# Performance work log

Measured on AMD Instinct MI355X. Metric: run time of the kernel, lower is better.

The kernel has to match this reference:

```python
import jax, jax.numpy as jnp
import numpy as np

NUM_BINS = 8
TAIL = 3.0
MBW = 0.001  # min_bin_width
MBH = 0.001  # min_bin_height
MD = 0.001   # min_derivative


def _conv(x, w, b):
    y = jax.lax.conv_general_dilated(x, w, (1, 1), 'SAME',
                                     dimension_numbers=('NCHW', 'OIHW', 'NCHW'))
    return y + b[None, :, None, None]


def _convnet(x, w1, b1, w2, b2, w3, b3):
    h = jax.nn.relu(_conv(x, w1, b1))
    h = jax.nn.relu(_conv(h, w2, b2))
    return _conv(h, w3, b3)


def _rqs_forward(x, uw, uh, ud):
    # x: (N,), uw/uh: (N, num_bins), ud: (N, num_bins-1)
    nb = uw.shape[-1]
    inside = (x >= -TAIL) & (x <= TAIL)
    xin = jnp.clip(x, -TAIL, TAIL)
    # linear tails: pad derivatives so boundary slope == 1
    const = float(np.log(np.exp(1.0 - MD) - 1.0))
    ud = jnp.pad(ud, ((0, 0), (1, 1)), constant_values=const)

    widths = jax.nn.softmax(uw, axis=-1)
    widths = MBW + (1.0 - MBW * nb) * widths
    cumw = jnp.pad(jnp.cumsum(widths, axis=-1), ((0, 0), (1, 0)))
    cumw = 2.0 * TAIL * cumw - TAIL
    cumw = cumw.at[:, 0].set(-TAIL).at[:, -1].set(TAIL)
    widths = cumw[:, 1:] - cumw[:, :-1]

    heights = jax.nn.softmax(uh, axis=-1)
    heights = MBH + (1.0 - MBH * nb) * heights
    cumh = jnp.pad(jnp.cumsum(heights, axis=-1), ((0, 0), (1, 0)))
    cumh = 2.0 * TAIL * cumh - TAIL
    cumh = cumh.at[:, 0].set(-TAIL).at[:, -1].set(TAIL)
    heights = cumh[:, 1:] - cumh[:, :-1]

    deriv = MD + jax.nn.softplus(ud)  # (N, nb+1)

    # searchsorted: locate bin of each element
    idx = jnp.clip(jnp.sum((xin[:, None] >= cumw).astype(jnp.int32), axis=-1) - 1, 0, nb - 1)
    gather = lambda t: jnp.take_along_axis(t, idx[:, None], axis=-1)[:, 0]

    in_cw = gather(cumw)
    in_w = gather(widths)
    in_ch = gather(cumh)
    in_h = gather(heights)
    in_delta = gather(heights / widths)
    d0 = gather(deriv)
    d1 = gather(deriv[:, 1:])

    theta = (xin - in_cw) / in_w
    tom = theta * (1.0 - theta)
    numer = in_h * (in_delta * theta ** 2 + d0 * tom)
    denom = in_delta + (d0 + d1 - 2.0 * in_delta) * tom
    y = in_ch + numer / denom
    dnum = in_delta ** 2 * (d1 * theta ** 2 + 2.0 * in_delta * tom + d0 * (1.0 - theta) ** 2)
    lad = jnp.log(dnum) - 2.0 * jnp.log(denom)

    y = jnp.where(inside, y, x)
    lad = jnp.where(inside, lad, 0.0)
    return y, lad


def setup_inputs() -> dict:
    key = jax.random.key(0)
    ks = jax.random.split(key, 9)
    B, C, H, W = 32, 12, 64, 64
    hidden = 128
    cond_c = C // 3
    out_spline = C * (3 * NUM_BINS - 1)
    x = jax.random.normal(ks[0], (B, C, H, W), dtype=jnp.float32)
    logdet = jnp.zeros((B,), dtype=jnp.float32)
    conditioning = jax.random.normal(ks[1], (B, cond_c, H, W), dtype=jnp.float32)
    w1 = jax.random.normal(ks[2], (hidden, C + cond_c, 3, 3), dtype=jnp.float32) * 0.05
    b1 = jnp.zeros((hidden,), dtype=jnp.float32)
    w2 = jax.random.normal(ks[3], (hidden, hidden, 1, 1), dtype=jnp.float32) * 0.05
    b2 = jnp.zeros((hidden,), dtype=jnp.float32)
    w3 = jax.random.normal(ks[4], (out_spline, hidden, 3, 3), dtype=jnp.float32) * 0.01
    b3 = jnp.zeros((out_spline,), dtype=jnp.float32)
    return {"x": x, "logdet": logdet, "conditioning": conditioning,
            "w1": w1, "b1": b1, "w2": w2, "b2": b2, "w3": w3, "b3": b3}


def reference(x, logdet, conditioning, w1, b1, w2, b2, w3, b3):
    B, C, H, W = x.shape
    net_in = jnp.concatenate([x, conditioning], axis=1)
    params = _convnet(net_in, w1, b1, w2, b2, w3, b3)  # (B, C*(3nb-1), H, W)
    params = params.reshape(B, C, 3 * NUM_BINS - 1, H, W)
    params = params.transpose(0, 1, 3, 4, 2).reshape(B * C * H * W, 3 * NUM_BINS - 1)
    uw = params[:, :NUM_BINS]
    uh = params[:, NUM_BINS:2 * NUM_BINS]
    ud = params[:, 2 * NUM_BINS:]
    y_flat, lad_flat = _rqs_forward(x.reshape(-1), uw, uh, ud)
    y = y_flat.reshape(B, C, H, W)
    logdet_out = logdet + lad_flat.reshape(B, -1).sum(axis=1)
    return y, logdet_out
```

## Files before the change

kernel.cpp:

```cpp
#include <hip/hip_runtime.h>
#include <math.h>


#define NY   1572864

typedef _Float16 half8 __attribute__((ext_vector_type(8)));
typedef _Float16 half4 __attribute__((ext_vector_type(4)));
typedef float f32x4 __attribute__((ext_vector_type(4)));

#define ASYNC16(gsrc, ldst) \
  __builtin_amdgcn_global_load_lds((const __attribute__((address_space(1))) unsigned int*)(gsrc), \
                                   (__attribute__((address_space(3))) unsigned int*)(ldst), 16, 0, 0)

#define H2P_PLANE 4356
#define H2P_IDX(b, cc, pp) ((((size_t)(b) * 4 + (cc)) * H2P_PLANE + (pp)) << 5)
#define XH_IDX(b, pp) (((size_t)(b) * H2P_PLANE + (pp)) << 5)

__global__ __launch_bounds__(256) void prep_xh_k(
    const float* __restrict__ w1, const float* __restrict__ w2,
    const float* __restrict__ w3, _Float16* __restrict__ w1h,
    _Float16* __restrict__ w2h, _Float16* __restrict__ w3h,
    const float* __restrict__ logdet, float* __restrict__ ld_out,
    const float* __restrict__ x, const float* __restrict__ cond,
    _Float16* __restrict__ xh, _Float16* __restrict__ h2p)
{
    const int i = blockIdx.x * 256 + threadIdx.x;
    if (i < 36864) {
        int k = i & 31, oc = (i >> 5) & 127, t = i >> 12;
        w1h[i] = (_Float16)((k < 16) ? w1[(oc * 16 + k) * 9 + t] : 0.f);
    }
    if (i < 16384) {
        int km = i & 31, oc = (i >> 5) & 127, ks = i >> 12;
        w2h[i] = (_Float16)w2[oc * 128 + ks * 32 + km];
    }
    {
        int cim = i & 31;
        int oc = (i >> 5) % 288;
        int tc = i / (288 * 32);
        int t = tc >> 2, cc = tc & 3;
        int c = oc / 24, j = oc % 24;
        int ci = cc * 32 + cim;
        float v = (j < 23) ? w3[((c * 23 + j) * 128 + ci) * 9 + t] : 0.f;
        w3h[i] = (_Float16)v;
    }
    if (i < 32) ld_out[i] = logdet[i];

    if (i < 133120) {
        const int q = i & 3;
        const int rest = i >> 2;
        const int r = rest % 260;
        const int cc2 = (rest / 260) & 3;
        const int bb = rest / 1040;
        int pp;
        if (r < 66)       pp = r;
        else if (r < 132) pp = 65 * 66 + (r - 66);
        else if (r < 196) pp = (r - 131) * 66;
        else              pp = (r - 195) * 66 + 65;
        f32x4 z = {0.f, 0.f, 0.f, 0.f};
        *(f32x4*)(h2p + H2P_IDX(bb, cc2, pp) + q * 8) = z;
    }

    if (i < 139392) {
        const int b = i / H2P_PLANE, pp = i % H2P_PLANE;
        const int pr = pp / 66, pc = pp % 66;
        const bool interior = (pr >= 1) && (pr <= 64) && (pc >= 1) && (pc <= 64);
        _Float16 v[32];
#pragma unroll
        for (int ci = 0; ci < 32; ++ci) v[ci] = (_Float16)0.f;
        if (interior) {
            const int p = (pr - 1) * 64 + (pc - 1);
#pragma unroll
            for (int ci = 0; ci < 12; ++ci)
                v[ci] = (_Float16)x[((size_t)(b * 12 + ci) << 12) + p];
#pragma unroll
            for (int ci = 0; ci < 4; ++ci)
                v[12 + ci] = (_Float16)cond[((size_t)(b * 4 + ci) << 12) + p];
        }
        _Float16* dst = xh + ((size_t)i << 5);
#pragma unroll
        for (int q = 0; q < 4; ++q) *(f32x4*)(dst + q * 8) = *(f32x4*)(v + q * 8);
    }
}

__global__ __launch_bounds__(256, 2) void conv12_k(
    const _Float16* __restrict__ xh, const _Float16* __restrict__ w1h,
    const _Float16* __restrict__ w2h, const float* __restrict__ b1,
    const float* __restrict__ b2, _Float16* __restrict__ h2p)
{
    __shared__ __align__(16) char smem[74240];
    float* b2l = (float*)(smem + 73728);
    _Float16* h1l = (_Float16*)smem;

    const int tid = threadIdx.x;
    const int wv = tid >> 6, lane = tid & 63;
    const int row16 = lane & 15, quad = lane >> 4;
    const int prow = wv >> 1, colb = (wv & 1) << 5;
    const int bid = blockIdx.x;
    const int b = bid >> 5;
    const int pim0 = (bid & 31) << 7;
    const int h0 = pim0 >> 6;

    if (tid < 128) b2l[tid] = b2[tid];
#pragma unroll
    for (int k = 0; k < 18; ++k)
        ASYNC16(w1h + (size_t)(k * 256 + tid) * 8, smem + (k * 256 + wv * 64) * 16);

    f32x4 acc[2][8];
#pragma unroll
    for (int pt = 0; pt < 2; ++pt)
#pragma unroll
        for (int ot = 0; ot < 8; ++ot) acc[pt][ot] = (f32x4){0.f, 0.f, 0.f, 0.f};

    __syncthreads();
    const _Float16* wl = (const _Float16*)smem;

    for (int t = 0; t < 9; ++t) {
        const int dy = t / 3, dx = t % 3;
        const int pbase = (h0 + prow + dy) * 66 + dx + colb + row16;
        half8 bf[2], af[8];
#pragma unroll
        for (int pt = 0; pt < 2; ++pt)
            bf[pt] = *(const half8*)(xh + XH_IDX(b, pbase + pt * 16) + quad * 8);
#pragma unroll
        for (int ot = 0; ot < 8; ++ot)
            af[ot] = *(const half8*)(wl + ((t * 128 + ot * 16 + row16) << 5) + quad * 8);
        __builtin_amdgcn_s_setprio(1);
#pragma unroll
        for (int ot = 0; ot < 8; ++ot)
#pragma unroll
            for (int pt = 0; pt < 2; ++pt)
                acc[pt][ot] = __builtin_amdgcn_mfma_f32_16x16x32_f16(af[ot], bf[pt], acc[pt][ot], 0, 0, 0);
        __builtin_amdgcn_s_setprio(0);
    }

    f32x4 bias[8];
#pragma unroll
    for (int ot = 0; ot < 8; ++ot) bias[ot] = *(const f32x4*)(b1 + ot * 16 + quad * 4);
    __syncthreads();

#pragma unroll
    for (int k = 0; k < 8; ++k)
        ASYNC16(w2h + (size_t)(k * 256 + tid) * 8, smem + 36864 + (k * 256 + wv * 64) * 16);

#pragma unroll
    for (int pt = 0; pt < 2; ++pt) {
        const int pix = wv * 32 + pt * 16 + row16;
#pragma unroll
        for (int ot = 0; ot < 8; ++ot) {
            half4 v;
#pragma unroll
            for (int r = 0; r < 4; ++r)
                v[r] = (_Float16)fmaxf(acc[pt][ot][r] + bias[ot][r], 0.f);
            *(half4*)(h1l + pix * 136 + ot * 16 + quad * 4) = v;
        }
    }
#pragma unroll
    for (int pt = 0; pt < 2; ++pt)
#pragma unroll
        for (int ot = 0; ot < 8; ++ot) acc[pt][ot] = (f32x4){0.f, 0.f, 0.f, 0.f};
    __syncthreads();

    const _Float16* w2l = (const _Float16*)(smem + 36864);
#pragma unroll
    for (int ks = 0; ks < 4; ++ks) {
        half8 bf[2], af[8];
#pragma unroll
        for (int pt = 0; pt < 2; ++pt)
            bf[pt] = *(const half8*)(h1l + (wv * 32 + pt * 16 + row16) * 136 + ks * 32 + quad * 8);
#pragma unroll
        for (int ot = 0; ot < 8; ++ot)
            af[ot] = *(const half8*)(w2l + ((ks * 128 + ot * 16 + row16) << 5) + quad * 8);
        __builtin_amdgcn_s_setprio(1);
#pragma unroll
        for (int ot = 0; ot < 8; ++ot)
#pragma unroll
            for (int pt = 0; pt < 2; ++pt)
                acc[pt][ot] = __builtin_amdgcn_mfma_f32_16x16x32_f16(af[ot], bf[pt], acc[pt][ot], 0, 0, 0);
        __builtin_amdgcn_s_setprio(0);
    }

#pragma unroll
    for (int pt = 0; pt < 2; ++pt) {
        const int p = pim0 + wv * 32 + pt * 16 + row16;
        const int pp = ((p >> 6) + 1) * 66 + (p & 63) + 1;
#pragma unroll
        for (int ot = 0; ot < 8; ++ot) {
            const int oc0 = ot * 16 + quad * 4;
            half4 v;
#pragma unroll
            for (int r = 0; r < 4; ++r)
                v[r] = (_Float16)fmaxf(acc[pt][ot][r] + b2l[oc0 + r], 0.f);
            *(half4*)(h2p + H2P_IDX(b, oc0 >> 5, pp) + (oc0 & 31)) = v;
        }
    }
}

__device__ __forceinline__ void rqs_eval(const f32x4* pv, float xv,
                                         float& yv_out, float& lad_out)
{
#define PRM(j) (pv[(j) >> 2][(j) & 3])
    const float xin = fminf(fmaxf(xv, -3.f), 3.f);

    float mw = PRM(0), mh = PRM(8);
#pragma unroll
    for (int j = 1; j < 8; ++j) { mw = fmaxf(mw, PRM(j)); mh = fmaxf(mh, PRM(8 + j)); }
    float ew[8], eh[8];
    float sw = 0.f, sh = 0.f;
#pragma unroll
    for (int j = 0; j < 8; ++j) {
        ew[j] = __expf(PRM(j) - mw);      sw += ew[j];
        eh[j] = __expf(PRM(8 + j) - mh);  sh += eh[j];
    }
    const float rw = 1.f / sw, rh = 1.f / sh;

    const float CONST_D = 0.5397423f;

    float cumw = 0.f, cumh = 0.f;
    float cw_lo = -3.f, ch_lo = -3.f;
    float in_cw = 0.f, in_w = 1.f, in_ch = 0.f, in_h = 1.f, sd0 = 0.f, sd1 = 0.f;
#pragma unroll
    for (int i = 0; i < 8; ++i) {
        cumw += fmaf(0.992f, ew[i] * rw, 0.001f);
        cumh += fmaf(0.992f, eh[i] * rh, 0.001f);
        const float cw_hi = (i == 7) ? 3.f : fmaf(6.f, cumw, -3.f);
        const float ch_hi = (i == 7) ? 3.f : fmaf(6.f, cumh, -3.f);
        const bool sel = (xin >= cw_lo) && ((i == 7) || (xin < cw_hi));
        in_cw = sel ? cw_lo : in_cw;
        in_w  = sel ? (cw_hi - cw_lo) : in_w;
        in_ch = sel ? ch_lo : in_ch;
        in_h  = sel ? (ch_hi - ch_lo) : in_h;
        sd0   = sel ? ((i == 0) ? CONST_D : PRM(16 + i - 1)) : sd0;
        sd1   = sel ? ((i == 7) ? CONST_D : PRM(16 + i)) : sd1;
        cw_lo = cw_hi; ch_lo = ch_hi;
    }

    const float d0 = 0.001f + ((sd0 > 20.f) ? sd0 : __logf(1.f + __expf(sd0)));
    const float d1 = 0.001f + ((sd1 > 20.f) ? sd1 : __logf(1.f + __expf(sd1)));

    const float r_inw = 1.f / in_w;
    const float delta = in_h * r_inw;
    const float theta = (xin - in_cw) * r_inw;
    const float omt = 1.f - theta;
    const float tom = theta * omt;
    const float th2 = theta * theta;
    const float numer = in_h * (delta * th2 + d0 * tom);
    const float denom = delta + (d0 + d1 - 2.f * delta) * tom;
    const float rden = 1.f / denom;
    float yv = in_ch + numer * rden;
    const float dnum = delta * delta * (d1 * th2 + 2.f * delta * tom + d0 * omt * omt);
    float lad = __logf(dnum * rden * rden);

    const bool inside = (xv >= -3.f) && (xv <= 3.f);
    yv_out = inside ? yv : xv;
    lad_out = inside ? lad : 0.f;
#undef PRM
}

__global__ __launch_bounds__(256, 2) void conv3_rqs_k(
    const _Float16* __restrict__ h2p, const _Float16* __restrict__ w3h,
    const float* __restrict__ b3, const float* __restrict__ x,
    float* __restrict__ y, float* __restrict__ ld_out)
{
    __shared__ __align__(16) char smem[81216];
    float* b3l = (float*)(smem + 80640);

    const int tid = threadIdx.x;
    const int wv = tid >> 6, lane = tid & 63;
    const int row16 = lane & 15, quad = lane >> 4;
    const int bid = blockIdx.x;
    const int g = bid >> 4, r = bid & 15;
    const int col = r >> 3;
    const int ptile = (g << 3) | (r & 7);
    const int b = ptile >> 4;
    const int pim0 = (ptile & 15) << 8;
    const int h0 = pim0 >> 6;

    if (tid < 144) {
        const int c = tid / 24, j = tid % 24;
        b3l[tid] = (j < 23) ? b3[(col * 6 + c) * 23 + j] : 0.f;
    }

    f32x4 acc[4][9];
#pragma unroll
    for (int pt = 0; pt < 4; ++pt)
#pragma unroll
        for (int ot = 0; ot < 9; ++ot) acc[pt][ot] = (f32x4){0.f, 0.f, 0.f, 0.f};

    auto stage_wt3 = [&](int dy, int cc, int buf) {
#pragma unroll
        for (int j = 0; j < 3; ++j) {
            const int t = dy * 3 + j;
            const _Float16* gp = w3h + ((size_t)((t * 4 + cc) * 288 + col * 144) << 5);
            char* wb = smem + 25344 + buf * 27648 + j * 9216;
            ASYNC16(gp + (size_t)tid * 8, wb + wv * 64 * 16);
            ASYNC16(gp + (size_t)(256 + tid) * 8, wb + (256 + wv * 64) * 16);
            if (wv == 0) ASYNC16(gp + (size_t)(512 + lane) * 8, wb + 512 * 16);
        }
    };
    auto stage_act = [&](int cc) {
        const _Float16* ga = h2p + H2P_IDX(b, cc, h0 * 66);
#pragma unroll
        for (int k = 0; k < 6; ++k)
            ASYNC16(ga + (size_t)(k * 256 + tid) * 8, smem + (k * 256 + wv * 64) * 16);
        if (wv == 0 && lane < 48)
            ASYNC16(ga + (size_t)(1536 + lane) * 8, smem + 1536 * 16);
    };

    stage_act(0);
    stage_wt3(0, 0, 0);

    for (int cc = 0; cc < 4; ++cc) {
        for (int dy = 0; dy < 3; ++dy) {
            const int step = cc * 3 + dy;
            __syncthreads();
            if (step + 1 < 12)
                stage_wt3((dy == 2) ? 0 : dy + 1, (dy == 2) ? cc + 1 : cc, (step + 1) & 1);
            const _Float16* act = (const _Float16*)smem;
            const _Float16* wt = (const _Float16*)(smem + 25344 + (step & 1) * 27648);
            const int lrow = (wv + dy) * 66 + row16;
#pragma unroll
            for (int dx = 0; dx < 3; ++dx) {
                half8 bf[4], af[9];
#pragma unroll
                for (int pt = 0; pt < 4; ++pt)
                    bf[pt] = *(const half8*)(act + ((lrow + dx + pt * 16) << 5) + quad * 8);
#pragma unroll
                for (int ot = 0; ot < 9; ++ot)
                    af[ot] = *(const half8*)(wt + dx * 4608 + ((ot * 16 + row16) << 5) + quad * 8);
#pragma unroll
                for (int ot = 0; ot < 9; ++ot)
#pragma unroll
                    for (int pt = 0; pt < 4; ++pt)
                        acc[pt][ot] = __builtin_amdgcn_mfma_f32_16x16x32_f16(af[ot], bf[pt], acc[pt][ot], 0, 0, 0);
            }
            if (dy == 2 && cc < 3) {
                __syncthreads();
                stage_act(cc + 1);
            }
        }
    }
    __syncthreads();

    float* epi = (float*)smem + wv * 4736;
    float lad_acc = 0.f;
#pragma unroll
    for (int ph = 0; ph < 2; ++ph) {
#pragma unroll
        for (int ptq = 0; ptq < 2; ++ptq)
#pragma unroll
            for (int ot = 0; ot < 9; ++ot)
                *(f32x4*)(epi + ptq * 2368 + row16 * 148 + ot * 16 + quad * 4)
                    = acc[ph * 2 + ptq][ot];
        asm volatile("s_waitcnt lgkmcnt(0)" ::: "memory");
        __builtin_amdgcn_sched_barrier(0);
#pragma unroll 1
        for (int pass = 0; pass < 3; ++pass) {
            const int idx = pass * 64 + lane;
            const int ptq = (idx >= 96) ? 1 : 0;
            const int rem = idx - ptq * 96;
            const int p16 = rem & 15, c = rem >> 4;
            const float* pb = epi + ptq * 2368 + p16 * 148 + c * 24;
            const float* bb = b3l + c * 24;
            f32x4 pv[6];
#pragma unroll
            for (int q = 0; q < 6; ++q)
                pv[q] = *(const f32x4*)(pb + q * 4) + *(const f32x4*)(bb + q * 4);
            const int tpix = wv * 64 + (ph * 2 + ptq) * 16 + p16;
            const size_t xi = (((size_t)(b * 12 + col * 6 + c)) << 12) + (pim0 + tpix);
            const float xv = x[xi];
            float yv, lad;
            rqs_eval(pv, xv, yv, lad);
            y[xi] = yv;
            lad_acc += lad;
        }
        asm volatile("s_waitcnt lgkmcnt(0)" ::: "memory");
        __builtin_amdgcn_sched_barrier(0);
    }

#pragma unroll
    for (int off = 32; off > 0; off >>= 1) lad_acc += __shfl_down(lad_acc, off);
    if (lane == 0) atomicAdd(&ld_out[b], lad_acc);
}

extern "C" void kernel_launch(void* const* d_in, const int* in_sizes, int n_in,
                              void* d_out, int out_size, void* d_ws, size_t ws_size,
                              hipStream_t stream)
{
    const float* x      = (const float*)d_in[0];
    const float* logdet = (const float*)d_in[1];
    const float* cond   = (const float*)d_in[2];
    const float* w1     = (const float*)d_in[3];
    const float* b1     = (const float*)d_in[4];
    const float* w2     = (const float*)d_in[5];
    const float* b2     = (const float*)d_in[6];
    const float* w3     = (const float*)d_in[7];
    const float* b3     = (const float*)d_in[8];

    char* ws = (char*)d_ws;
    _Float16* xh  = (_Float16*)ws;
    _Float16* h2p = (_Float16*)(ws + 33554432);
    _Float16* w1h = (_Float16*)(ws + 69238784);
    _Float16* w2h = (_Float16*)(ws + 69312512);
    _Float16* w3h = (_Float16*)(ws + 69345280);

    float* y      = (float*)d_out;
    float* ld_out = y + NY;

    prep_xh_k<<<1296, 256, 0, stream>>>(w1, w2, w3, w1h, w2h, w3h, logdet, ld_out, x, cond, xh, h2p);
    conv12_k<<<1024, 256, 0, stream>>>(xh, w1h, w2h, b1, b2, h2p);
    conv3_rqs_k<<<1024, 256, 0, stream>>>(h2p, w3h, b3, x, y, ld_out);
}
```

Measured before the change: 200.2 us.

## Pack two conv1 taps per MFMA K-slice and shrink padded input layout

Measured after the change: 194.2 us. 1.03x faster.

```diff
diff --git a/kernel.cpp b/kernel.cpp
--- a/kernel.cpp
+++ b/kernel.cpp
@@ -14,20 +14,27 @@
 
 #define H2P_PLANE 4356
 #define H2P_IDX(b, cc, pp) ((((size_t)(b) * 4 + (cc)) * H2P_PLANE + (pp)) << 5)
-#define XH_IDX(b, pp) (((size_t)(b) * H2P_PLANE + (pp)) << 5)
+#define XH_IDX(b, pp) (((size_t)(b) * H2P_PLANE + (pp)) << 4)
 
 __global__ __launch_bounds__(256) void prep_xh_k(
     const float* __restrict__ w1, const float* __restrict__ w2,
-    const float* __restrict__ w3, _Float16* __restrict__ w1h,
+    const float* __restrict__ w3, _Float16* __restrict__ w1p,
     _Float16* __restrict__ w2h, _Float16* __restrict__ w3h,
     const float* __restrict__ logdet, float* __restrict__ ld_out,
     const float* __restrict__ x, const float* __restrict__ cond,
     _Float16* __restrict__ xh, _Float16* __restrict__ h2p)
 {
     const int i = blockIdx.x * 256 + threadIdx.x;
-    if (i < 36864) {
-        int k = i & 31, oc = (i >> 5) & 127, t = i >> 12;
-        w1h[i] = (_Float16)((k < 16) ? w1[(oc * 16 + k) * 9 + t] : 0.f);
+    if (i < 20480) {
+        int k = i & 31, oc = (i >> 5) & 127, s = i >> 12;
+        float v;
+        if (s < 4) {
+            int t = 2 * s + (k >> 4), ci = k & 15;
+            v = w1[(oc * 16 + ci) * 9 + t];
+        } else {
+            v = (k < 16) ? w1[(oc * 16 + k) * 9 + 8] : 0.f;
+        }
+        w1p[i] = (_Float16)v;
     }
     if (i < 16384) {
         int km = i & 31, oc = (i >> 5) & 127, ks = i >> 12;
@@ -64,9 +71,9 @@
         const int b = i / H2P_PLANE, pp = i % H2P_PLANE;
         const int pr = pp / 66, pc = pp % 66;
         const bool interior = (pr >= 1) && (pr <= 64) && (pc >= 1) && (pc <= 64);
-        _Float16 v[32];
-#pragma unroll
-        for (int ci = 0; ci < 32; ++ci) v[ci] = (_Float16)0.f;
+        _Float16 v[16];
+#pragma unroll
+        for (int ci = 0; ci < 16; ++ci) v[ci] = (_Float16)0.f;
         if (interior) {
             const int p = (pr - 1) * 64 + (pc - 1);
 #pragma unroll
@@ -76,14 +83,14 @@
             for (int ci = 0; ci < 4; ++ci)
                 v[12 + ci] = (_Float16)cond[((size_t)(b * 4 + ci) << 12) + p];
         }
-        _Float16* dst = xh + ((size_t)i << 5);
-#pragma unroll
-        for (int q = 0; q < 4; ++q) *(f32x4*)(dst + q * 8) = *(f32x4*)(v + q * 8);
+        _Float16* dst = xh + ((size_t)i << 4);
+#pragma unroll
+        for (int q = 0; q < 2; ++q) *(f32x4*)(dst + q * 8) = *(f32x4*)(v + q * 8);
     }
 }
 
 __global__ __launch_bounds__(256, 2) void conv12_k(
-    const _Float16* __restrict__ xh, const _Float16* __restrict__ w1h,
+    const _Float16* __restrict__ xh, const _Float16* __restrict__ w1p,
     const _Float16* __restrict__ w2h, const float* __restrict__ b1,
     const float* __restrict__ b2, _Float16* __restrict__ h2p)
 {
@@ -102,8 +109,11 @@
 
     if (tid < 128) b2l[tid] = b2[tid];
 #pragma unroll
-    for (int k = 0; k < 18; ++k)
-        ASYNC16(w1h + (size_t)(k * 256 + tid) * 8, smem + (k * 256 + wv * 64) * 16);
+    for (int k = 0; k < 10; ++k)
+        ASYNC16(w1p + (size_t)(k * 256 + tid) * 8, smem + (k * 256 + wv * 64) * 16);
+#pragma unroll
+    for (int k = 0; k < 8; ++k)
+        ASYNC16(w2h + (size_t)(k * 256 + tid) * 8, smem + 40960 + (k * 256 + wv * 64) * 16);
 
     f32x4 acc[2][8];
 #pragma unroll
@@ -114,16 +124,23 @@
     __syncthreads();
     const _Float16* wl = (const _Float16*)smem;
 
-    for (int t = 0; t < 9; ++t) {
-        const int dy = t / 3, dx = t % 3;
-        const int pbase = (h0 + prow + dy) * 66 + dx + colb + row16;
+#pragma unroll
+    for (int s = 0; s < 5; ++s) {
+        const int t0 = 2 * s;
+        const int t1 = (s < 4) ? 2 * s + 1 : 2 * s;
+        const int dy0 = t0 / 3, dx0 = t0 % 3;
+        const int dy1 = t1 / 3, dx1 = t1 % 3;
+        const int pb0 = (h0 + prow + dy0) * 66 + dx0 + colb + row16;
+        const int pb1 = (h0 + prow + dy1) * 66 + dx1 + colb + row16;
+        const int pbq = (quad < 2) ? pb0 : pb1;
+        const int koff = (quad & 1) * 8;
         half8 bf[2], af[8];
 #pragma unroll
         for (int pt = 0; pt < 2; ++pt)
-            bf[pt] = *(const half8*)(xh + XH_IDX(b, pbase + pt * 16) + quad * 8);
+            bf[pt] = *(const half8*)(xh + XH_IDX(b, pbq + pt * 16) + koff);
 #pragma unroll
         for (int ot = 0; ot < 8; ++ot)
-            af[ot] = *(const half8*)(wl + ((t * 128 + ot * 16 + row16) << 5) + quad * 8);
+            af[ot] = *(const half8*)(wl + ((s * 128 + ot * 16 + row16) << 5) + quad * 8);
         __builtin_amdgcn_s_setprio(1);
 #pragma unroll
         for (int ot = 0; ot < 8; ++ot)
@@ -139,10 +156,6 @@
     __syncthreads();
 
 #pragma unroll
-    for (int k = 0; k < 8; ++k)
-        ASYNC16(w2h + (size_t)(k * 256 + tid) * 8, smem + 36864 + (k * 256 + wv * 64) * 16);
-
-#pragma unroll
     for (int pt = 0; pt < 2; ++pt) {
         const int pix = wv * 32 + pt * 16 + row16;
 #pragma unroll
@@ -160,7 +173,7 @@
         for (int ot = 0; ot < 8; ++ot) acc[pt][ot] = (f32x4){0.f, 0.f, 0.f, 0.f};
     __syncthreads();
 
-    const _Float16* w2l = (const _Float16*)(smem + 36864);
+    const _Float16* w2l = (const _Float16*)(smem + 40960);
 #pragma unroll
     for (int ks = 0; ks < 4; ++ks) {
         half8 bf[2], af[8];
@@ -399,14 +412,14 @@
     char* ws = (char*)d_ws;
     _Float16* xh  = (_Float16*)ws;
     _Float16* h2p = (_Float16*)(ws + 33554432);
-    _Float16* w1h = (_Float16*)(ws + 69238784);
+    _Float16* w1p = (_Float16*)(ws + 69238784);
     _Float16* w2h = (_Float16*)(ws + 69312512);
     _Float16* w3h = (_Float16*)(ws + 69345280);
 
     float* y      = (float*)d_out;
     float* ld_out = y + NY;
 
-    prep_xh_k<<<1296, 256, 0, stream>>>(w1, w2, w3, w1h, w2h, w3h, logdet, ld_out, x, cond, xh, h2p);
-    conv12_k<<<1024, 256, 0, stream>>>(xh, w1h, w2h, b1, b2, h2p);
+    prep_xh_k<<<1296, 256, 0, stream>>>(w1, w2, w3, w1p, w2h, w3h, logdet, ld_out, x, cond, xh, h2p);
+    conv12_k<<<1024, 256, 0, stream>>>(xh, w1p, w2h, b1, b2, h2p);
     conv3_rqs_k<<<1024, 256, 0, stream>>>(h2p, w3h, b3, x, y, ld_out);
 }
```
